# Kernel optimization log

Hardware: AMD Instinct MI355X
Metric: run time of the kernel (lower is better)

The kernel has to match this reference:

```python
import jax, jax.numpy as jnp
import numpy as np

N_ITEM = 100_000
N_USER = 100_000
IN_DIM = 128
OUT_DIM = 128
H = 8
DK = OUT_DIM // H  # 16
SQRT_DK = DK ** 0.5
NODE_DICT = {"item": 0, "user": 1}
# canonical etypes: (src_ntype, dst_ntype, relation_id)
ETYPES = [("item", "user", 0), ("item", "user", 1), ("user", "item", 2)]
N_NODES = {"item": N_ITEM, "user": N_USER}
N_EDGES = [500_000, 250_000, 250_000]


def _seg_softmax(scores, seg, n):
    # edge_softmax over incoming edges of each dst node, per head
    m = jax.ops.segment_max(scores, seg, num_segments=n)
    m = jnp.where(jnp.isfinite(m), m, 0.0)  # empty segments
    e = jnp.exp(scores - m[seg])
    s = jax.ops.segment_sum(e, seg, num_segments=n)
    return e / s[seg]


def _forward(h_item, h_user, Wk, bk, Wq, bq, Wv, bv, Wa, ba,
             rel_pri, rel_att, rel_msg, skip, edge_lists):
    h = {"item": h_item, "user": h_user}
    agg = {"item": [], "user": []}
    for (src, dst, r), (se, de) in zip(ETYPES, edge_lists):
        sid, did = NODE_DICT[src], NODE_DICT[dst]
        # relation-specific K/V bilinear transforms
        k = (h[src] @ Wk[sid] + bk[sid]).reshape(-1, H, DK)
        k = jnp.einsum('nhd,hde->nhe', k, rel_att[r])
        v = (h[src] @ Wv[sid] + bv[sid]).reshape(-1, H, DK)
        v = jnp.einsum('nhd,hde->nhe', v, rel_msg[r])
        q = (h[dst] @ Wq[did] + bq[did]).reshape(-1, H, DK)
        # per-edge dot-product attention (v_dot_u)
        att = jnp.einsum('ehd,ehd->eh', q[de], k[se]) * rel_pri[r] / SQRT_DK
        att = _seg_softmax(att, de, N_NODES[dst])
        # u_mul_e + sum aggregation
        t = jax.ops.segment_sum(v[se] * att[:, :, None], de, num_segments=N_NODES[dst])
        agg[dst].append(t)
    outs = []
    for ntype in ["item", "user"]:
        nid = NODE_DICT[ntype]
        # cross_reducer='mean' across etypes landing on this ntype
        t = sum(agg[ntype]) / float(len(agg[ntype]))
        t = t.reshape(-1, OUT_DIM)
        trans = t @ Wa[nid] + ba[nid]  # dropout disabled (eval)
        alpha = jax.nn.sigmoid(skip[nid])
        outs.append(trans * alpha + h[ntype] * (1.0 - alpha))
    return jnp.stack(outs)  # [2, 100000, 128] (item, user)


def setup_inputs() -> dict:
    key = jax.random.key(0)
    ks = jax.random.split(key, 20)
    w_s = (1.0 / IN_DIM) ** 0.5
    xav = (6.0 / (DK + DK)) ** 0.5
    inp = {
        "h_item": jax.random.normal(ks[0], (N_ITEM, IN_DIM), dtype=jnp.float32),
        "h_user": jax.random.normal(ks[1], (N_USER, IN_DIM), dtype=jnp.float32),
        "Wk": jax.random.normal(ks[2], (2, IN_DIM, OUT_DIM), dtype=jnp.float32) * w_s,
        "bk": jax.random.normal(ks[3], (2, OUT_DIM), dtype=jnp.float32) * 0.01,
        "Wq": jax.random.normal(ks[4], (2, IN_DIM, OUT_DIM), dtype=jnp.float32) * w_s,
        "bq": jax.random.normal(ks[5], (2, OUT_DIM), dtype=jnp.float32) * 0.01,
        "Wv": jax.random.normal(ks[6], (2, IN_DIM, OUT_DIM), dtype=jnp.float32) * w_s,
        "bv": jax.random.normal(ks[7], (2, OUT_DIM), dtype=jnp.float32) * 0.01,
        "Wa": jax.random.normal(ks[8], (2, OUT_DIM, OUT_DIM), dtype=jnp.float32) * w_s,
        "ba": jax.random.normal(ks[9], (2, OUT_DIM), dtype=jnp.float32) * 0.01,
        "rel_pri": jnp.ones((3, H), dtype=jnp.float32),
        "rel_att": jax.random.uniform(ks[10], (3, H, DK, DK), minval=-xav, maxval=xav, dtype=jnp.float32),
        "rel_msg": jax.random.uniform(ks[11], (3, H, DK, DK), minval=-xav, maxval=xav, dtype=jnp.float32),
        "skip": jnp.ones((2,), dtype=jnp.float32),
        "click_src": jax.random.randint(ks[12], (N_EDGES[0],), 0, N_ITEM),
        "click_dst": jax.random.randint(ks[13], (N_EDGES[0],), 0, N_USER),
        "purchase_src": jax.random.randint(ks[14], (N_EDGES[1],), 0, N_ITEM),
        "purchase_dst": jax.random.randint(ks[15], (N_EDGES[1],), 0, N_USER),
        "rev_src": jax.random.randint(ks[16], (N_EDGES[2],), 0, N_USER),
        "rev_dst": jax.random.randint(ks[17], (N_EDGES[2],), 0, N_ITEM),
    }
    return inp


def reference(h_item, h_user, Wk, bk, Wq, bq, Wv, bv, Wa, ba,
              rel_pri, rel_att, rel_msg, skip,
              click_src, click_dst, purchase_src, purchase_dst, rev_src, rev_dst):
    edge_lists = [(click_src, click_dst), (purchase_src, purchase_dst), (rev_src, rev_dst)]
    return _forward(h_item, h_user, Wk, bk, Wq, bq, Wv, bv, Wa, ba,
                    rel_pri, rel_att, rel_msg, skip, edge_lists)
```

## Files before the change

### kernel.cpp

```cpp
#include <hip/hip_runtime.h>
#include <math.h>

#define NN 100000
#define NM ((size_t)NN * 128)

__global__ void prep_weights(
    const float* __restrict__ Wk, const float* __restrict__ bk,
    const float* __restrict__ Wq, const float* __restrict__ bq,
    const float* __restrict__ Wv, const float* __restrict__ bv,
    const float* __restrict__ Wa, const float* __restrict__ rel_pri,
    const float* __restrict__ rel_att, const float* __restrict__ rel_msg,
    float* __restrict__ B_item, float* __restrict__ bias_item,
    float* __restrict__ B_user, float* __restrict__ bias_user,
    float* __restrict__ Wfin)
{
    int t = blockIdx.x * 256 + threadIdx.x;

    if (t < 128 * 384) {
        int k = t / 384, c = t % 384;
        float v;
        if (c < 128)      v = Wk[k * 128 + c];
        else if (c < 256) v = Wv[k * 128 + (c - 128)];
        else {
            int cc = c - 256, h = cc >> 4, d = cc & 15;
            const float* A = rel_att + 2 * 2048 + h * 256 + d * 16;
            const float* w = Wq + k * 128 + h * 16;
            float s = 0.f;
            #pragma unroll
            for (int e = 0; e < 16; ++e) s += w[e] * A[e];
            v = s * (rel_pri[16 + h] * 0.25f);
        }
        B_item[k * 384 + c] = v;
        return;
    }
    t -= 128 * 384;
    if (t < 384) {
        int c = t; float v;
        if (c < 128)      v = bk[c];
        else if (c < 256) v = bv[c - 128];
        else {
            int cc = c - 256, h = cc >> 4, d = cc & 15;
            const float* A = rel_att + 2 * 2048 + h * 256 + d * 16;
            const float* b = bq + h * 16;
            float s = 0.f;
            #pragma unroll
            for (int e = 0; e < 16; ++e) s += b[e] * A[e];
            v = s * (rel_pri[16 + h] * 0.25f);
        }
        bias_item[c] = v;
        return;
    }
    t -= 384;
    if (t < 128 * 512) {
        int k = t / 512, c = t % 512;
        float v;
        if (c < 128)      v = Wk[16384 + k * 128 + c];
        else if (c < 256) v = Wv[16384 + k * 128 + (c - 128)];
        else {
            int rr = (c < 384) ? 0 : 1;
            int cc = (c - 256) & 127, h = cc >> 4, d = cc & 15;
            const float* A = rel_att + rr * 2048 + h * 256 + d * 16;
            const float* w = Wq + 16384 + k * 128 + h * 16;
            float s = 0.f;
            #pragma unroll
            for (int e = 0; e < 16; ++e) s += w[e] * A[e];
            v = s * (rel_pri[rr * 8 + h] * 0.25f);
        }
        B_user[k * 512 + c] = v;
        return;
    }
    t -= 128 * 512;
    if (t < 512) {
        int c = t; float v;
        if (c < 128)      v = bk[128 + c];
        else if (c < 256) v = bv[128 + c - 128];
        else {
            int rr = (c < 384) ? 0 : 1;
            int cc = (c - 256) & 127, h = cc >> 4, d = cc & 15;
            const float* A = rel_att + rr * 2048 + h * 256 + d * 16;
            const float* b = bq + 128 + h * 16;
            float s = 0.f;
            #pragma unroll
            for (int e = 0; e < 16; ++e) s += b[e] * A[e];
            v = s * (rel_pri[rr * 8 + h] * 0.25f);
        }
        bias_user[c] = v;
        return;
    }
    t -= 512;
    if (t < 3 * 16384) {
        int which = t / 16384, rem = t % 16384;
        int rin = rem / 128, c = rem % 128;
        int h = rin >> 4, d = rin & 15;
        const float* M; const float* W; float scale;
        if (which == 0)      { M = rel_msg + 2 * 2048 + h * 256 + d * 16; W = Wa;         scale = 1.0f; }
        else if (which == 1) { M = rel_msg + 0        + h * 256 + d * 16; W = Wa + 16384; scale = 0.5f; }
        else                 { M = rel_msg + 2048     + h * 256 + d * 16; W = Wa + 16384; scale = 0.5f; }
        float s = 0.f;
        #pragma unroll
        for (int e = 0; e < 16; ++e) s += M[e] * W[(h * 16 + e) * 128 + c];
        Wfin[which * 16384 + rin * 128 + c] = s * scale;
    }
}

struct OutPtrs { float* p[4]; };

__global__ __launch_bounds__(256) void gemm_node(
    const float* __restrict__ A, const float* __restrict__ B,
    const float* __restrict__ bias, OutPtrs outs, int M, int Bstride)
{
    __shared__ float Bs[16 * 128];
    __shared__ float As[128 * 16];
    const int tid = threadIdx.x;
    const int gy = blockIdx.y;
    const int tile = blockIdx.x;
    const int tx = tid & 15, ty = tid >> 4;

    float acc[8][8];
    #pragma unroll
    for (int i = 0; i < 8; ++i)
        #pragma unroll
        for (int j = 0; j < 8; ++j) acc[i][j] = 0.f;

    for (int ks = 0; ks < 128; ks += 16) {
        __syncthreads();
        #pragma unroll
        for (int it = 0; it < 2; ++it) {
            int f = tid + it * 256;
            int k = f >> 5, lc4 = f & 31;
            *(float4*)(Bs + k * 128 + lc4 * 4) =
                *(const float4*)(B + (size_t)(ks + k) * Bstride + gy * 128 + lc4 * 4);
        }
        #pragma unroll
        for (int it = 0; it < 2; ++it) {
            int f = tid + it * 256;
            int row = f >> 2, kk4 = f & 3;
            int r = tile * 128 + row;
            float4 v = make_float4(0.f, 0.f, 0.f, 0.f);
            if (r < M) v = *(const float4*)(A + (size_t)r * 128 + ks + kk4 * 4);
            *(float4*)(As + row * 16 + kk4 * 4) = v;
        }
        __syncthreads();
        #pragma unroll
        for (int kk = 0; kk < 16; ++kk) {
            float4 b0 = *(const float4*)(Bs + kk * 128 + tx * 4);
            float4 b1 = *(const float4*)(Bs + kk * 128 + 64 + tx * 4);
            #pragma unroll
            for (int i = 0; i < 8; ++i) {
                float a = As[(ty + 16 * i) * 16 + kk];
                acc[i][0] += a * b0.x; acc[i][1] += a * b0.y;
                acc[i][2] += a * b0.z; acc[i][3] += a * b0.w;
                acc[i][4] += a * b1.x; acc[i][5] += a * b1.y;
                acc[i][6] += a * b1.z; acc[i][7] += a * b1.w;
            }
        }
    }

    float4 bi0 = *(const float4*)(bias + gy * 128 + tx * 4);
    float4 bi1 = *(const float4*)(bias + gy * 128 + 64 + tx * 4);
    float* out = outs.p[gy];
    #pragma unroll
    for (int i = 0; i < 8; ++i) {
        int r = tile * 128 + ty + 16 * i;
        if (r < M) {
            float4 o0 = make_float4(acc[i][0] + bi0.x, acc[i][1] + bi0.y,
                                    acc[i][2] + bi0.z, acc[i][3] + bi0.w);
            float4 o1 = make_float4(acc[i][4] + bi1.x, acc[i][5] + bi1.y,
                                    acc[i][6] + bi1.z, acc[i][7] + bi1.w);
            *(float4*)(out + (size_t)r * 128 + tx * 4) = o0;
            *(float4*)(out + (size_t)r * 128 + 64 + tx * 4) = o1;
        }
    }
}

__global__ __launch_bounds__(256) void gemm_final(
    const float* A0, const float* A1,
    const float* __restrict__ B0, const float* B1,
    const float* __restrict__ ba, const float* __restrict__ skipv, int nid,
    const float* __restrict__ hin, float* out, int M)
{
    __shared__ float Bs[16 * 128];
    __shared__ float As[128 * 16];
    const int tid = threadIdx.x;
    const int tile = blockIdx.x;
    const int tx = tid & 15, ty = tid >> 4;

    float acc[8][8];
    #pragma unroll
    for (int i = 0; i < 8; ++i)
        #pragma unroll
        for (int j = 0; j < 8; ++j) acc[i][j] = 0.f;

    const float* Ap[2] = { A0, A1 };
    const float* Bp[2] = { B0, B1 };
    const int nA = (A1 != nullptr) ? 2 : 1;

    for (int p = 0; p < nA; ++p) {
        const float* Acur = Ap[p];
        const float* Bcur = Bp[p];
        for (int ks = 0; ks < 128; ks += 16) {
            __syncthreads();
            #pragma unroll
            for (int it = 0; it < 2; ++it) {
                int f = tid + it * 256;
                int k = f >> 5, lc4 = f & 31;
                *(float4*)(Bs + k * 128 + lc4 * 4) =
                    *(const float4*)(Bcur + (size_t)(ks + k) * 128 + lc4 * 4);
            }
            #pragma unroll
            for (int it = 0; it < 2; ++it) {
                int f = tid + it * 256;
                int row = f >> 2, kk4 = f & 3;
                int r = tile * 128 + row;
                float4 v = make_float4(0.f, 0.f, 0.f, 0.f);
                if (r < M) v = *(const float4*)(Acur + (size_t)r * 128 + ks + kk4 * 4);
                *(float4*)(As + row * 16 + kk4 * 4) = v;
            }
            __syncthreads();
            #pragma unroll
            for (int kk = 0; kk < 16; ++kk) {
                float4 b0 = *(const float4*)(Bs + kk * 128 + tx * 4);
                float4 b1 = *(const float4*)(Bs + kk * 128 + 64 + tx * 4);
                #pragma unroll
                for (int i = 0; i < 8; ++i) {
                    float a = As[(ty + 16 * i) * 16 + kk];
                    acc[i][0] += a * b0.x; acc[i][1] += a * b0.y;
                    acc[i][2] += a * b0.z; acc[i][3] += a * b0.w;
                    acc[i][4] += a * b1.x; acc[i][5] += a * b1.y;
                    acc[i][6] += a * b1.z; acc[i][7] += a * b1.w;
                }
            }
        }
    }

    float sv = skipv[nid];
    float alpha = 1.f / (1.f + __expf(-sv));
    float beta = 1.f - alpha;
    float4 ba0 = *(const float4*)(ba + tx * 4);
    float4 ba1 = *(const float4*)(ba + 64 + tx * 4);
    #pragma unroll
    for (int i = 0; i < 8; ++i) {
        int r = tile * 128 + ty + 16 * i;
        if (r < M) {
            float4 h0 = *(const float4*)(hin + (size_t)r * 128 + tx * 4);
            float4 h1 = *(const float4*)(hin + (size_t)r * 128 + 64 + tx * 4);
            float4 o0 = make_float4((acc[i][0] + ba0.x) * alpha + h0.x * beta,
                                    (acc[i][1] + ba0.y) * alpha + h0.y * beta,
                                    (acc[i][2] + ba0.z) * alpha + h0.z * beta,
                                    (acc[i][3] + ba0.w) * alpha + h0.w * beta);
            float4 o1 = make_float4((acc[i][4] + ba1.x) * alpha + h1.x * beta,
                                    (acc[i][5] + ba1.y) * alpha + h1.y * beta,
                                    (acc[i][6] + ba1.z) * alpha + h1.z * beta,
                                    (acc[i][7] + ba1.w) * alpha + h1.w * beta);
            *(float4*)(out + (size_t)r * 128 + tx * 4) = o0;
            *(float4*)(out + (size_t)r * 128 + 64 + tx * 4) = o1;
        }
    }
}

__global__ void zero_int(int* __restrict__ p, int n) {
    int i = blockIdx.x * 256 + threadIdx.x;
    if (i < n) p[i] = 0;
}
__global__ void hist3(const int* __restrict__ d0, const int* __restrict__ d1,
                      const int* __restrict__ d2, int E0, int E1, int E2,
                      int* __restrict__ cnt) {
    int e = blockIdx.x * 256 + threadIdx.x;
    int g;
    if (e < E0) g = 0 * NN + d0[e];
    else if (e < E0 + E1) g = 1 * NN + d1[e - E0];
    else if (e < E0 + E1 + E2) g = 2 * NN + d2[e - E0 - E1];
    else return;
    atomicAdd(&cnt[g], 1);
}
__global__ void scan1(const int* __restrict__ cnt, int* __restrict__ offs,
                      int* __restrict__ psum, int n) {
    __shared__ int sm[1024];
    int t = threadIdx.x, i = blockIdx.x * 1024 + t;
    int v = (i < n) ? cnt[i] : 0;
    sm[t] = v; __syncthreads();
    for (int off = 1; off < 1024; off <<= 1) {
        int x = (t >= off) ? sm[t - off] : 0;
        __syncthreads();
        sm[t] += x;
        __syncthreads();
    }
    if (i < n) offs[i] = sm[t] - v;
    if (t == 1023) psum[blockIdx.x] = sm[1023];
}
__global__ void scan2(int* __restrict__ psum, int nb) {
    __shared__ int sm[512];
    int t = threadIdx.x;
    int v = (t < nb) ? psum[t] : 0;
    sm[t] = v; __syncthreads();
    for (int off = 1; off < 512; off <<= 1) {
        int x = (t >= off) ? sm[t - off] : 0;
        __syncthreads();
        sm[t] += x;
        __syncthreads();
    }
    if (t < nb) psum[t] = sm[t] - v;
}
__global__ void scan3(int* __restrict__ offs, const int* __restrict__ psum, int n) {
    int i = blockIdx.x * 256 + threadIdx.x;
    if (i < n) offs[i] += psum[i >> 10];
}
__global__ void scatter3(const int* __restrict__ s0, const int* __restrict__ d0,
                         const int* __restrict__ s1, const int* __restrict__ d1,
                         const int* __restrict__ s2, const int* __restrict__ d2,
                         int E0, int E1, int E2,
                         const int* __restrict__ offs, int* __restrict__ pos,
                         int* __restrict__ csrc) {
    int e = blockIdx.x * 256 + threadIdx.x;
    int g, s;
    if (e < E0) { g = 0 * NN + d0[e]; s = s0[e]; }
    else if (e < E0 + E1) { int l = e - E0; g = 1 * NN + d1[l]; s = s1[l]; }
    else if (e < E0 + E1 + E2) { int l = e - E0 - E1; g = 2 * NN + d2[l]; s = s2[l]; }
    else return;
    int p = atomicAdd(&pos[g], 1);
    csrc[offs[g] + p] = s;
}

__global__ __launch_bounds__(256) void edge_attn(
    const float* qt, const float* __restrict__ kb, const float* __restrict__ vb,
    const int* __restrict__ offs, const int* __restrict__ deg,
    const int* __restrict__ csrc, float* aggout)
{
    int g = blockIdx.x * 32 + (threadIdx.x >> 3);
    int h = threadIdx.x & 7;
    if (g >= NN) return;

    const float* qrow = qt + (size_t)g * 128 + h * 16;
    float4 q0 = *(const float4*)(qrow);
    float4 q1 = *(const float4*)(qrow + 4);
    float4 q2 = *(const float4*)(qrow + 8);
    float4 q3 = *(const float4*)(qrow + 12);

    int s = offs[g], dg = deg[g];
    float m = -__builtin_inff(), sum = 0.f;
    float4 a0 = make_float4(0, 0, 0, 0), a1 = a0, a2 = a0, a3 = a0;

    for (int e = 0; e < dg; ++e) {
        int src = csrc[s + e];
        const float* krow = kb + (size_t)src * 128 + h * 16;
        float4 k0 = *(const float4*)(krow);
        float4 k1 = *(const float4*)(krow + 4);
        float4 k2 = *(const float4*)(krow + 8);
        float4 k3 = *(const float4*)(krow + 12);
        float sc = q0.x * k0.x + q0.y * k0.y + q0.z * k0.z + q0.w * k0.w
                 + q1.x * k1.x + q1.y * k1.y + q1.z * k1.z + q1.w * k1.w
                 + q2.x * k2.x + q2.y * k2.y + q2.z * k2.z + q2.w * k2.w
                 + q3.x * k3.x + q3.y * k3.y + q3.z * k3.z + q3.w * k3.w;
        float mn = fmaxf(m, sc);
        float cr = __expf(m - mn);
        float w = __expf(sc - mn);
        sum = sum * cr + w;
        m = mn;
        const float* vrow = vb + (size_t)src * 128 + h * 16;
        float4 v0 = *(const float4*)(vrow);
        float4 v1 = *(const float4*)(vrow + 4);
        float4 v2 = *(const float4*)(vrow + 8);
        float4 v3 = *(const float4*)(vrow + 12);
        a0.x = a0.x * cr + w * v0.x; a0.y = a0.y * cr + w * v0.y;
        a0.z = a0.z * cr + w * v0.z; a0.w = a0.w * cr + w * v0.w;
        a1.x = a1.x * cr + w * v1.x; a1.y = a1.y * cr + w * v1.y;
        a1.z = a1.z * cr + w * v1.z; a1.w = a1.w * cr + w * v1.w;
        a2.x = a2.x * cr + w * v2.x; a2.y = a2.y * cr + w * v2.y;
        a2.z = a2.z * cr + w * v2.z; a2.w = a2.w * cr + w * v2.w;
        a3.x = a3.x * cr + w * v3.x; a3.y = a3.y * cr + w * v3.y;
        a3.z = a3.z * cr + w * v3.z; a3.w = a3.w * cr + w * v3.w;
    }

    float inv = (dg > 0) ? 1.f / sum : 0.f;
    float* orow = aggout + (size_t)g * 128 + h * 16;
    a0.x *= inv; a0.y *= inv; a0.z *= inv; a0.w *= inv;
    a1.x *= inv; a1.y *= inv; a1.z *= inv; a1.w *= inv;
    a2.x *= inv; a2.y *= inv; a2.z *= inv; a2.w *= inv;
    a3.x *= inv; a3.y *= inv; a3.z *= inv; a3.w *= inv;
    *(float4*)(orow) = a0;
    *(float4*)(orow + 4) = a1;
    *(float4*)(orow + 8) = a2;
    *(float4*)(orow + 12) = a3;
}

extern "C" void kernel_launch(void* const* d_in, const int* in_sizes, int n_in,
                              void* d_out, int out_size, void* d_ws, size_t ws_size,
                              hipStream_t stream)
{
    const float* h_item = (const float*)d_in[0];
    const float* h_user = (const float*)d_in[1];
    const float* Wk  = (const float*)d_in[2];
    const float* bk  = (const float*)d_in[3];
    const float* Wq  = (const float*)d_in[4];
    const float* bq  = (const float*)d_in[5];
    const float* Wv  = (const float*)d_in[6];
    const float* bv  = (const float*)d_in[7];
    const float* Wa  = (const float*)d_in[8];
    const float* ba  = (const float*)d_in[9];
    const float* rel_pri = (const float*)d_in[10];
    const float* rel_att = (const float*)d_in[11];
    const float* rel_msg = (const float*)d_in[12];
    const float* skipv   = (const float*)d_in[13];
    const int* s0 = (const int*)d_in[14]; const int* d0 = (const int*)d_in[15];
    const int* s1 = (const int*)d_in[16]; const int* d1 = (const int*)d_in[17];
    const int* s2 = (const int*)d_in[18]; const int* d2 = (const int*)d_in[19];
    const int E0 = in_sizes[14], E1 = in_sizes[16], E2 = in_sizes[18];
    const int Etot = E0 + E1 + E2;

    float* ws = (float*)d_ws;
    float* kb_i = ws;
    float* vb_i = ws + NM;
    float* kb_u = ws + 2 * NM;
    float* vb_u = ws + 3 * NM;
    float* qt1  = ws + 4 * NM;
    float* wreg = ws + 5 * NM;
    float* B_item    = wreg;
    float* bias_item = wreg + 49152;
    float* B_user    = wreg + 49536;
    float* bias_user = wreg + 115072;
    float* Wfin      = wreg + 115584;
    int* ibuf = (int*)(wreg + 115584 + 49152);
    int* cnt  = ibuf;
    int* pos  = ibuf + 3 * NN;
    int* offs = ibuf + 6 * NN;
    int* psum = ibuf + 9 * NN;
    int* csrc = ibuf + 9 * NN + 512;

    float* out_item = (float*)d_out;
    float* out_user = (float*)d_out + NM;

    prep_weights<<<644, 256, 0, stream>>>(Wk, bk, Wq, bq, Wv, bv, Wa, rel_pri,
                                          rel_att, rel_msg,
                                          B_item, bias_item, B_user, bias_user, Wfin);

    const int tiles = (NN + 127) / 128;
    OutPtrs oi; oi.p[0] = kb_i; oi.p[1] = vb_i; oi.p[2] = out_item; oi.p[3] = nullptr;
    OutPtrs ou; ou.p[0] = kb_u; ou.p[1] = vb_u; ou.p[2] = out_user; ou.p[3] = qt1;
    gemm_node<<<dim3(tiles, 3), 256, 0, stream>>>(h_item, B_item, bias_item, oi, NN, 384);
    gemm_node<<<dim3(tiles, 4), 256, 0, stream>>>(h_user, B_user, bias_user, ou, NN, 512);

    zero_int<<<(6 * NN + 255) / 256, 256, 0, stream>>>(ibuf, 6 * NN);
    hist3<<<(Etot + 255) / 256, 256, 0, stream>>>(d0, d1, d2, E0, E1, E2, cnt);
    const int nscan = 3 * NN;
    const int nb1024 = (nscan + 1023) / 1024;
    scan1<<<nb1024, 1024, 0, stream>>>(cnt, offs, psum, nscan);
    scan2<<<1, 512, 0, stream>>>(psum, nb1024);
    scan3<<<(nscan + 255) / 256, 256, 0, stream>>>(offs, psum, nscan);
    scatter3<<<(Etot + 255) / 256, 256, 0, stream>>>(s0, d0, s1, d1, s2, d2,
                                                     E0, E1, E2, offs, pos, csrc);

    const int gblocks = (NN + 31) / 32;
    edge_attn<<<gblocks, 256, 0, stream>>>(out_user, kb_i, vb_i,
                                           offs,          cnt,          csrc, out_user);
    edge_attn<<<gblocks, 256, 0, stream>>>(qt1,      kb_i, vb_i,
                                           offs + NN,     cnt + NN,     csrc, qt1);
    edge_attn<<<gblocks, 256, 0, stream>>>(out_item, kb_u, vb_u,
                                           offs + 2 * NN, cnt + 2 * NN, csrc, out_item);

    gemm_final<<<tiles, 256, 0, stream>>>(out_item, nullptr, Wfin, nullptr,
                                          ba, skipv, 0, h_item, out_item, NN);
    gemm_final<<<tiles, 256, 0, stream>>>(out_user, qt1, Wfin + 16384, Wfin + 2 * 16384,
                                          ba + 128, skipv, 1, h_user, out_user, NN);
}
```

Measured before the change: 1.023 ms.

## Merge per-type launches into batched grids and widen GEMM K-tile

The two node-projection GEMMs, the three per-relation edge-attention launches and the two final GEMMs each become a single launch, with blockIdx.y selecting the pointer set from a parameter struct. The shared GEMM body now stages a K-slice of 32 instead of 16 in LDS, pads the A tile to a row stride of 36, and reads A as float4 in groups of four k values. The intent is to cut launch count and tail effects and to halve the number of barriers per tile. In exchange, LDS per block roughly doubles, which may lower occupancy, and the item and user final GEMMs now share one grid despite doing unequal amounts of work.

```diff
diff --git a/kernel.cpp b/kernel.cpp
--- a/kernel.cpp
+++ b/kernel.cpp
@@ -103,18 +103,69 @@
     }
 }
 
-struct OutPtrs { float* p[4]; };
-
-__global__ __launch_bounds__(256) void gemm_node(
-    const float* __restrict__ A, const float* __restrict__ B,
-    const float* __restrict__ bias, OutPtrs outs, int M, int Bstride)
+#define GEMM_TILE_BODY(BPTR, BSTRIDE, APTR)                                    \
+    for (int ks = 0; ks < 128; ks += 32) {                                     \
+        __syncthreads();                                                       \
+        _Pragma("unroll")                                                      \
+        for (int it = 0; it < 4; ++it) {                                       \
+            int f = tid + it * 256;                                            \
+            int k = f >> 5, lc4 = f & 31;                                      \
+            *(float4*)(Bs + k * 128 + lc4 * 4) =                               \
+                *(const float4*)(BPTR + (size_t)(ks + k) * BSTRIDE + lc4 * 4); \
+        }                                                                      \
+        _Pragma("unroll")                                                      \
+        for (int it = 0; it < 4; ++it) {                                       \
+            int f = tid + it * 256;                                            \
+            int row = f >> 3, kk4 = f & 7;                                     \
+            int r = tile * 128 + row;                                          \
+            float4 v = make_float4(0.f, 0.f, 0.f, 0.f);                        \
+            if (r < NN) v = *(const float4*)(APTR + (size_t)r * 128 + ks + kk4 * 4); \
+            *(float4*)(As + row * 36 + kk4 * 4) = v;                           \
+        }                                                                      \
+        __syncthreads();                                                       \
+        _Pragma("unroll")                                                      \
+        for (int kq = 0; kq < 8; ++kq) {                                       \
+            float a4[8][4];                                                    \
+            _Pragma("unroll")                                                  \
+            for (int i = 0; i < 8; ++i)                                        \
+                *(float4*)a4[i] = *(const float4*)(As + (ty + 16 * i) * 36 + kq * 4); \
+            _Pragma("unroll")                                                  \
+            for (int j = 0; j < 4; ++j) {                                      \
+                int kk = kq * 4 + j;                                           \
+                float4 b0 = *(const float4*)(Bs + kk * 128 + tx * 4);          \
+                float4 b1 = *(const float4*)(Bs + kk * 128 + 64 + tx * 4);     \
+                _Pragma("unroll")                                              \
+                for (int i = 0; i < 8; ++i) {                                  \
+                    float a = a4[i][j];                                        \
+                    acc[i][0] += a * b0.x; acc[i][1] += a * b0.y;              \
+                    acc[i][2] += a * b0.z; acc[i][3] += a * b0.w;              \
+                    acc[i][4] += a * b1.x; acc[i][5] += a * b1.y;              \
+                    acc[i][6] += a * b1.z; acc[i][7] += a * b1.w;              \
+                }                                                              \
+            }                                                                  \
+        }                                                                      \
+    }
+
+struct NodeParams {
+    const float* A[7];
+    const float* Bcol[7];
+    const float* biasc[7];
+    float* out[7];
+    int stride[7];
+};
+
+__global__ __launch_bounds__(256) void gemm_node(NodeParams P)
 {
-    __shared__ float Bs[16 * 128];
-    __shared__ float As[128 * 16];
+    __shared__ float Bs[32 * 128];
+    __shared__ float As[128 * 36];
     const int tid = threadIdx.x;
     const int gy = blockIdx.y;
     const int tile = blockIdx.x;
     const int tx = tid & 15, ty = tid >> 4;
+
+    const float* A = P.A[gy];
+    const float* B = P.Bcol[gy];
+    const int Bstride = P.stride[gy];
 
     float acc[8][8];
     #pragma unroll
@@ -122,47 +173,16 @@
         #pragma unroll
         for (int j = 0; j < 8; ++j) acc[i][j] = 0.f;
 
-    for (int ks = 0; ks < 128; ks += 16) {
-        __syncthreads();
-        #pragma unroll
-        for (int it = 0; it < 2; ++it) {
-            int f = tid + it * 256;
-            int k = f >> 5, lc4 = f & 31;
-            *(float4*)(Bs + k * 128 + lc4 * 4) =
-                *(const float4*)(B + (size_t)(ks + k) * Bstride + gy * 128 + lc4 * 4);
-        }
-        #pragma unroll
-        for (int it = 0; it < 2; ++it) {
-            int f = tid + it * 256;
-            int row = f >> 2, kk4 = f & 3;
-            int r = tile * 128 + row;
-            float4 v = make_float4(0.f, 0.f, 0.f, 0.f);
-            if (r < M) v = *(const float4*)(A + (size_t)r * 128 + ks + kk4 * 4);
-            *(float4*)(As + row * 16 + kk4 * 4) = v;
-        }
-        __syncthreads();
-        #pragma unroll
-        for (int kk = 0; kk < 16; ++kk) {
-            float4 b0 = *(const float4*)(Bs + kk * 128 + tx * 4);
-            float4 b1 = *(const float4*)(Bs + kk * 128 + 64 + tx * 4);
-            #pragma unroll
-            for (int i = 0; i < 8; ++i) {
-                float a = As[(ty + 16 * i) * 16 + kk];
-                acc[i][0] += a * b0.x; acc[i][1] += a * b0.y;
-                acc[i][2] += a * b0.z; acc[i][3] += a * b0.w;
-                acc[i][4] += a * b1.x; acc[i][5] += a * b1.y;
-                acc[i][6] += a * b1.z; acc[i][7] += a * b1.w;
-            }
-        }
-    }
-
-    float4 bi0 = *(const float4*)(bias + gy * 128 + tx * 4);
-    float4 bi1 = *(const float4*)(bias + gy * 128 + 64 + tx * 4);
-    float* out = outs.p[gy];
+    GEMM_TILE_BODY(B, Bstride, A)
+
+    const float* bias = P.biasc[gy];
+    float4 bi0 = *(const float4*)(bias + tx * 4);
+    float4 bi1 = *(const float4*)(bias + 64 + tx * 4);
+    float* out = P.out[gy];
     #pragma unroll
     for (int i = 0; i < 8; ++i) {
         int r = tile * 128 + ty + 16 * i;
-        if (r < M) {
+        if (r < NN) {
             float4 o0 = make_float4(acc[i][0] + bi0.x, acc[i][1] + bi0.y,
                                     acc[i][2] + bi0.z, acc[i][3] + bi0.w);
             float4 o1 = make_float4(acc[i][4] + bi1.x, acc[i][5] + bi1.y,
@@ -173,15 +193,19 @@
     }
 }
 
-__global__ __launch_bounds__(256) void gemm_final(
-    const float* A0, const float* A1,
-    const float* __restrict__ B0, const float* B1,
-    const float* __restrict__ ba, const float* __restrict__ skipv, int nid,
-    const float* __restrict__ hin, float* out, int M)
+struct FinParams {
+    const float* A0[2]; const float* A1[2];
+    const float* B0[2]; const float* B1[2];
+    const float* ba[2]; const float* hin[2];
+    float* out[2];
+};
+
+__global__ __launch_bounds__(256) void gemm_final(FinParams P, const float* __restrict__ skipv)
 {
-    __shared__ float Bs[16 * 128];
-    __shared__ float As[128 * 16];
+    __shared__ float Bs[32 * 128];
+    __shared__ float As[128 * 36];
     const int tid = threadIdx.x;
+    const int gy = blockIdx.y;
     const int tile = blockIdx.x;
     const int tx = tid & 15, ty = tid >> 4;
 
@@ -191,57 +215,28 @@
         #pragma unroll
         for (int j = 0; j < 8; ++j) acc[i][j] = 0.f;
 
-    const float* Ap[2] = { A0, A1 };
-    const float* Bp[2] = { B0, B1 };
-    const int nA = (A1 != nullptr) ? 2 : 1;
+    const float* Ap[2] = { P.A0[gy], P.A1[gy] };
+    const float* Bp[2] = { P.B0[gy], P.B1[gy] };
+    const int nA = (Ap[1] != nullptr) ? 2 : 1;
 
     for (int p = 0; p < nA; ++p) {
         const float* Acur = Ap[p];
         const float* Bcur = Bp[p];
-        for (int ks = 0; ks < 128; ks += 16) {
-            __syncthreads();
-            #pragma unroll
-            for (int it = 0; it < 2; ++it) {
-                int f = tid + it * 256;
-                int k = f >> 5, lc4 = f & 31;
-                *(float4*)(Bs + k * 128 + lc4 * 4) =
-                    *(const float4*)(Bcur + (size_t)(ks + k) * 128 + lc4 * 4);
-            }
-            #pragma unroll
-            for (int it = 0; it < 2; ++it) {
-                int f = tid + it * 256;
-                int row = f >> 2, kk4 = f & 3;
-                int r = tile * 128 + row;
-                float4 v = make_float4(0.f, 0.f, 0.f, 0.f);
-                if (r < M) v = *(const float4*)(Acur + (size_t)r * 128 + ks + kk4 * 4);
-                *(float4*)(As + row * 16 + kk4 * 4) = v;
-            }
-            __syncthreads();
-            #pragma unroll
-            for (int kk = 0; kk < 16; ++kk) {
-                float4 b0 = *(const float4*)(Bs + kk * 128 + tx * 4);
-                float4 b1 = *(const float4*)(Bs + kk * 128 + 64 + tx * 4);
-                #pragma unroll
-                for (int i = 0; i < 8; ++i) {
-                    float a = As[(ty + 16 * i) * 16 + kk];
-                    acc[i][0] += a * b0.x; acc[i][1] += a * b0.y;
-                    acc[i][2] += a * b0.z; acc[i][3] += a * b0.w;
-                    acc[i][4] += a * b1.x; acc[i][5] += a * b1.y;
-                    acc[i][6] += a * b1.z; acc[i][7] += a * b1.w;
-                }
-            }
-        }
-    }
-
-    float sv = skipv[nid];
+        GEMM_TILE_BODY(Bcur, 128, Acur)
+    }
+
+    float sv = skipv[gy];
     float alpha = 1.f / (1.f + __expf(-sv));
     float beta = 1.f - alpha;
+    const float* ba = P.ba[gy];
+    const float* hin = P.hin[gy];
+    float* out = P.out[gy];
     float4 ba0 = *(const float4*)(ba + tx * 4);
     float4 ba1 = *(const float4*)(ba + 64 + tx * 4);
     #pragma unroll
     for (int i = 0; i < 8; ++i) {
         int r = tile * 128 + ty + 16 * i;
-        if (r < M) {
+        if (r < NN) {
             float4 h0 = *(const float4*)(hin + (size_t)r * 128 + tx * 4);
             float4 h1 = *(const float4*)(hin + (size_t)r * 128 + 64 + tx * 4);
             float4 o0 = make_float4((acc[i][0] + ba0.x) * alpha + h0.x * beta,
@@ -321,14 +316,25 @@
     csrc[offs[g] + p] = s;
 }
 
+struct EdgeParams {
+    const float* qt[3];
+    const float* kb[3];
+    const float* vb[3];
+    float* agg[3];
+};
+
 __global__ __launch_bounds__(256) void edge_attn(
-    const float* qt, const float* __restrict__ kb, const float* __restrict__ vb,
-    const int* __restrict__ offs, const int* __restrict__ deg,
-    const int* __restrict__ csrc, float* aggout)
+    EdgeParams P, const int* __restrict__ offs, const int* __restrict__ deg,
+    const int* __restrict__ csrc)
 {
+    int r = blockIdx.y;
     int g = blockIdx.x * 32 + (threadIdx.x >> 3);
     int h = threadIdx.x & 7;
     if (g >= NN) return;
+
+    const float* qt = P.qt[r];
+    const float* kb = P.kb[r];
+    const float* vb = P.vb[r];
 
     const float* qrow = qt + (size_t)g * 128 + h * 16;
     float4 q0 = *(const float4*)(qrow);
@@ -336,7 +342,7 @@
     float4 q2 = *(const float4*)(qrow + 8);
     float4 q3 = *(const float4*)(qrow + 12);
 
-    int s = offs[g], dg = deg[g];
+    int s = offs[r * NN + g], dg = deg[r * NN + g];
     float m = -__builtin_inff(), sum = 0.f;
     float4 a0 = make_float4(0, 0, 0, 0), a1 = a0, a2 = a0, a3 = a0;
 
@@ -372,7 +378,7 @@
     }
 
     float inv = (dg > 0) ? 1.f / sum : 0.f;
-    float* orow = aggout + (size_t)g * 128 + h * 16;
+    float* orow = P.agg[r] + (size_t)g * 128 + h * 16;
     a0.x *= inv; a0.y *= inv; a0.z *= inv; a0.w *= inv;
     a1.x *= inv; a1.y *= inv; a1.z *= inv; a1.w *= inv;
     a2.x *= inv; a2.y *= inv; a2.z *= inv; a2.w *= inv;
@@ -434,10 +440,19 @@
                                           B_item, bias_item, B_user, bias_user, Wfin);
 
     const int tiles = (NN + 127) / 128;
-    OutPtrs oi; oi.p[0] = kb_i; oi.p[1] = vb_i; oi.p[2] = out_item; oi.p[3] = nullptr;
-    OutPtrs ou; ou.p[0] = kb_u; ou.p[1] = vb_u; ou.p[2] = out_user; ou.p[3] = qt1;
-    gemm_node<<<dim3(tiles, 3), 256, 0, stream>>>(h_item, B_item, bias_item, oi, NN, 384);
-    gemm_node<<<dim3(tiles, 4), 256, 0, stream>>>(h_user, B_user, bias_user, ou, NN, 512);
+
+    NodeParams np;
+    for (int gy = 0; gy < 3; ++gy) {
+        np.A[gy] = h_item; np.Bcol[gy] = B_item + gy * 128;
+        np.biasc[gy] = bias_item + gy * 128; np.stride[gy] = 384;
+    }
+    for (int gy = 3; gy < 7; ++gy) {
+        np.A[gy] = h_user; np.Bcol[gy] = B_user + (gy - 3) * 128;
+        np.biasc[gy] = bias_user + (gy - 3) * 128; np.stride[gy] = 512;
+    }
+    np.out[0] = kb_i; np.out[1] = vb_i; np.out[2] = out_item;
+    np.out[3] = kb_u; np.out[4] = vb_u; np.out[5] = out_user; np.out[6] = qt1;
+    gemm_node<<<dim3(tiles, 7), 256, 0, stream>>>(np);
 
     zero_int<<<(6 * NN + 255) / 256, 256, 0, stream>>>(ibuf, 6 * NN);
     hist3<<<(Etot + 255) / 256, 256, 0, stream>>>(d0, d1, d2, E0, E1, E2, cnt);
@@ -449,16 +464,18 @@
     scatter3<<<(Etot + 255) / 256, 256, 0, stream>>>(s0, d0, s1, d1, s2, d2,
                                                      E0, E1, E2, offs, pos, csrc);
 
-    const int gblocks = (NN + 31) / 32;
-    edge_attn<<<gblocks, 256, 0, stream>>>(out_user, kb_i, vb_i,
-                                           offs,          cnt,          csrc, out_user);
-    edge_attn<<<gblocks, 256, 0, stream>>>(qt1,      kb_i, vb_i,
-                                           offs + NN,     cnt + NN,     csrc, qt1);
-    edge_attn<<<gblocks, 256, 0, stream>>>(out_item, kb_u, vb_u,
-                                           offs + 2 * NN, cnt + 2 * NN, csrc, out_item);
-
-    gemm_final<<<tiles, 256, 0, stream>>>(out_item, nullptr, Wfin, nullptr,
-                                          ba, skipv, 0, h_item, out_item, NN);
-    gemm_final<<<tiles, 256, 0, stream>>>(out_user, qt1, Wfin + 16384, Wfin + 2 * 16384,
-                                          ba + 128, skipv, 1, h_user, out_user, NN);
-}
+    EdgeParams ep;
+    ep.qt[0] = out_user; ep.kb[0] = kb_i; ep.vb[0] = vb_i; ep.agg[0] = out_user;
+    ep.qt[1] = qt1;      ep.kb[1] = kb_i; ep.vb[1] = vb_i; ep.agg[1] = qt1;
+    ep.qt[2] = out_item; ep.kb[2] = kb_u; ep.vb[2] = vb_u; ep.agg[2] = out_item;
+    edge_attn<<<dim3((NN + 31) / 32, 3), 256, 0, stream>>>(ep, offs, cnt, csrc);
+
+    FinParams fp;
+    fp.A0[0] = out_item; fp.A1[0] = nullptr;
+    fp.B0[0] = Wfin;     fp.B1[0] = nullptr;
+    fp.ba[0] = ba;       fp.hin[0] = h_item; fp.out[0] = out_item;
+    fp.A0[1] = out_user; fp.A1[1] = qt1;
+    fp.B0[1] = Wfin + 16384; fp.B1[1] = Wfin + 2 * 16384;
+    fp.ba[1] = ba + 128; fp.hin[1] = h_user; fp.out[1] = out_user;
+    gemm_final<<<dim3(tiles, 2), 256, 0, stream>>>(fp, skipv);
+}
```

New measurement: 992.3 us. 3.0% less time.
